# Kernel optimization log

Measured on AMD Instinct MI355X. Metric: run time of the kernel, lower is better.

The kernel has to match this reference:

```python
import jax, jax.numpy as jnp
import numpy as np

N = 50000       # nodes
E = 500000      # edges (before self-loops)
F_IN = 128      # node feature dim
F_E = 16        # edge feature dim
H = 8           # heads (conv1, conv2)
C1 = 32         # 256 // 8
C2 = 16         # 128 // 8
OUT = 1         # conv3 output channels (1 head, concat=False)
NS = 0.2        # leaky_relu negative slope
EPS = 1e-5      # batchnorm eps


def setup_inputs() -> dict:
    key = jax.random.key(0)
    ks = jax.random.split(key, 32)
    r = lambda k, s: jax.random.normal(k, s, jnp.float32) * 0.1
    inp = {
        'x': jax.random.normal(ks[0], (N, F_IN), jnp.float32),
        'edge_index': jax.random.randint(ks[1], (2, E), 0, N, jnp.int32),
        'edge_attr': jax.random.normal(ks[2], (E, F_E), jnp.float32),
        # conv1 (share_weights=True -> single lin)
        'W1': r(ks[3], (F_IN, H * C1)), 'b1': jnp.zeros((H * C1,), jnp.float32),
        'We1': r(ks[4], (F_E, H * C1)), 'att1': r(ks[5], (H, C1)),
        'bo1': jnp.zeros((H * C1,), jnp.float32),
        'g1': jnp.ones((H * C1,), jnp.float32), 'bt1': jnp.zeros((H * C1,), jnp.float32),
        # conv2 (share_weights=True)
        'W2': r(ks[6], (H * C1, H * C2)), 'b2': jnp.zeros((H * C2,), jnp.float32),
        'We2': r(ks[7], (F_E, H * C2)), 'att2': r(ks[8], (H, C2)),
        'bo2': jnp.zeros((H * C2,), jnp.float32),
        'g2': jnp.ones((H * C2,), jnp.float32), 'bt2': jnp.zeros((H * C2,), jnp.float32),
        # conv3 (share_weights=False -> separate lin_l / lin_r; 1 head, concat=False)
        'W3l': r(ks[9], (H * C2, OUT)), 'b3l': jnp.zeros((OUT,), jnp.float32),
        'W3r': r(ks[10], (H * C2, OUT)), 'b3r': jnp.zeros((OUT,), jnp.float32),
        'We3': r(ks[11], (F_E, OUT)), 'att3': r(ks[12], (1, OUT)),
        'bo3': jnp.zeros((OUT,), jnp.float32),
    }
    return inp


def _gatv2(x, src, dst, eattr, Wl, bl, Wr, br, We, att, bo, heads, ch, concat):
    """One GATv2Conv layer (PyG semantics), edges already include self-loops."""
    n = x.shape[0]
    xl = (x @ Wl + bl).reshape(n, heads, ch)              # source transform
    xr = (x @ Wr + br).reshape(n, heads, ch)              # target transform
    e = (eattr @ We).reshape(-1, heads, ch)               # edge transform (no bias)
    m = xl[src] + xr[dst] + e                             # [Etot, H, C]
    logit = jnp.einsum('ehc,hc->eh', jax.nn.leaky_relu(m, NS), att)
    lmax = jax.ops.segment_max(logit, dst, num_segments=n)
    ex = jnp.exp(logit - lmax[dst])
    denom = jax.ops.segment_sum(ex, dst, num_segments=n)
    alpha = ex / (denom[dst] + 1e-16)                     # segment softmax over dst
    out = jax.ops.segment_sum(alpha[:, :, None] * xl[src], dst, num_segments=n)
    out = out.reshape(n, heads * ch) if concat else out.mean(axis=1)
    return out + bo


def _bn(x, g, b):
    mu = x.mean(axis=0)
    var = ((x - mu) ** 2).mean(axis=0)
    return g * (x - mu) * jax.lax.rsqrt(var + EPS) + b


def reference(x, edge_index, edge_attr, W1, b1, We1, att1, bo1, g1, bt1,
              W2, b2, We2, att2, bo2, g2, bt2,
              W3l, b3l, W3r, b3r, We3, att3, bo3):
    n = x.shape[0]
    # add_self_loops=True with fill_value='mean' for edge_attr (PyG default)
    loop = jnp.arange(n, dtype=edge_index.dtype)
    src = jnp.concatenate([edge_index[0], loop])
    dst = jnp.concatenate([edge_index[1], loop])
    ea = jnp.concatenate([edge_attr,
                          jnp.broadcast_to(edge_attr.mean(axis=0), (n, edge_attr.shape[1]))], axis=0)

    h = _gatv2(x, src, dst, ea, W1, b1, W1, b1, We1, att1, bo1, H, C1, True)
    h = jax.nn.elu(_bn(h, g1, bt1))
    h = _gatv2(h, src, dst, ea, W2, b2, W2, b2, We2, att2, bo2, H, C2, True)
    h = jax.nn.elu(_bn(h, g2, bt2))
    out = _gatv2(h, src, dst, ea, W3l, b3l, W3r, b3r, We3, att3, bo3, 1, OUT, False)
    return out  # [N, 1]
```

## Files before the change

kernel.cpp:

```cpp
#include <hip/hip_runtime.h>

typedef unsigned short u16;
typedef __attribute__((ext_vector_type(4))) float f32x4;
typedef __attribute__((ext_vector_type(2))) float f32x2;
typedef __attribute__((ext_vector_type(8))) short bf16x8;

constexpr int Nn  = 50000;
constexpr int Ee  = 500000;
constexpr int ET  = Nn + Ee;
constexpr int FIN = 128;
constexpr int FE  = 16;
constexpr int Hh  = 8;
constexpr int C1  = 32, HC1 = 256;
constexpr int C2  = 16, HC2 = 128;
constexpr float NS  = 0.2f;
constexpr float EPS = 1e-5f;

__device__ __forceinline__ float b2f(u16 u) { return __uint_as_float(((unsigned)u) << 16); }
__device__ __forceinline__ u16 f2b(float f) {
  unsigned u = __float_as_uint(f);
  u += 0x7FFF + ((u >> 16) & 1);
  return (u16)(u >> 16);
}
__device__ __forceinline__ f32x2 ldbf2(const u16* p) {
  ushort2 u = *reinterpret_cast<const ushort2*>(p);
  return (f32x2){b2f(u.x), b2f(u.y)};
}
__device__ __forceinline__ void stbf2(u16* p, f32x2 v) {
  ushort2 u; u.x = f2b(v.x); u.y = f2b(v.y);
  *reinterpret_cast<ushort2*>(p) = u;
}

__global__ void k_init(int* __restrict__ deg, int* __restrict__ cursor, float* __restrict__ ea_mean,
                       float* __restrict__ bn1s, float* __restrict__ bn1q,
                       float* __restrict__ bn2s, float* __restrict__ bn2q) {
  int t = blockIdx.x * 256 + threadIdx.x;
  int stride = gridDim.x * 256;
  for (int i = t; i < Nn; i += stride) { deg[i] = 0; cursor[i] = 0; }
  if (t < FE) ea_mean[t] = 0.f;
  if (t >= 64 && t < 64 + HC1) { bn1s[t - 64] = 0.f; bn1q[t - 64] = 0.f; }
  if (t >= 384 && t < 384 + HC2) { bn2s[t - 384] = 0.f; bn2q[t - 384] = 0.f; }
}

__global__ void k_deg_mean(const int* __restrict__ ei, const float* __restrict__ ea,
                           int* __restrict__ deg, float* __restrict__ ea_mean) {
  int t = threadIdx.x;
  int e = blockIdx.x * 256 + t;
  if (e < ET) {
    int d = (e < Ee) ? ei[Ee + e] : (e - Ee);
    if ((unsigned)d >= (unsigned)Nn) d = 0;
    atomicAdd(&deg[d], 1);
  }
  __shared__ float s[256];
  int f  = t & 15;
  int r0 = (t >> 4) + blockIdx.x * 16;
  float acc = 0.f;
  for (int r = r0; r < Ee; r += gridDim.x * 16) acc += ea[r * FE + f];
  s[t] = acc;
  __syncthreads();
  if (t < 16) {
    float v = 0.f;
    for (int r = 0; r < 16; r++) v += s[r * 16 + t];
    atomicAdd(&ea_mean[t], v * (1.f / Ee));
  }
}

__global__ __launch_bounds__(1024) void k_scan(const int* __restrict__ deg, int* __restrict__ rowptr) {
  const int T = 1024;
  int t = threadIdx.x;
  const int CH = (Nn + T - 1) / T;
  int base = t * CH;
  int sum = 0;
  for (int i = 0; i < CH; i++) {
    int idx = base + i;
    if (idx < Nn) sum += deg[idx];
  }
  __shared__ int s[T];
  s[t] = sum;
  __syncthreads();
  for (int off = 1; off < T; off <<= 1) {
    int v = (t >= off) ? s[t - off] : 0;
    __syncthreads();
    s[t] += v;
    __syncthreads();
  }
  int run = (t == 0) ? 0 : s[t - 1];
  for (int i = 0; i < CH; i++) {
    int idx = base + i;
    if (idx < Nn) { rowptr[idx] = run; run += deg[idx]; }
  }
  if (t == T - 1) rowptr[Nn] = run;
}

__global__ void k_scatter(const int* __restrict__ ei, const int* __restrict__ rowptr,
                          int* __restrict__ cursor, int2* __restrict__ epack) {
  int e = blockIdx.x * 256 + threadIdx.x;
  if (e >= ET) return;
  int s, d;
  if (e < Ee) { s = ei[e]; d = ei[Ee + e]; } else { s = d = e - Ee; }
  if ((unsigned)s >= (unsigned)Nn) s = 0;
  if ((unsigned)d >= (unsigned)Nn) d = 0;
  int pos = rowptr[d] + atomicAdd(&cursor[d], 1);
  epack[pos] = make_int2(s, e);
}

__global__ void k_bn_coef(const float* __restrict__ sum, const float* __restrict__ sq,
                          const float* __restrict__ g, const float* __restrict__ bt,
                          float2* __restrict__ coef, int HC) {
  int ch = threadIdx.x;
  if (ch >= HC) return;
  float mu = sum[ch] * (1.f / Nn);
  float var = sq[ch] * (1.f / Nn) - mu * mu;
  float rs = rsqrtf(var + EPS);
  float sc = g[ch] * rs;
  coef[ch] = make_float2(sc, bt[ch] - sc * mu);
}

template <int HC>
__global__ void k_bn_stats(const u16* __restrict__ x, float* __restrict__ sum, float* __restrict__ sq) {
  long e0 = (long)blockIdx.x * 256 + threadIdx.x;
  long stride = (long)gridDim.x * 256;
  float s = 0.f, s2 = 0.f;
  for (long e = e0; e < (long)Nn * HC; e += stride) {
    float v = b2f(x[e]);
    s += v; s2 += v * v;
  }
  int ch = (int)(e0 % HC);
  atomicAdd(&sum[ch], s);
  atomicAdd(&sq[ch], s2);
}

template <int KK, int NN, typename AT, bool FUSE>
__global__ __launch_bounds__(256) void k_gemm_mfma(const AT* __restrict__ A, const float* __restrict__ W,
                                                   const float* __restrict__ bias, u16* __restrict__ C,
                                                   const float2* __restrict__ coef, int M) {
  constexpr int WT = KK + 8;
  __shared__ u16 Wt[64 * WT];
  int tid = threadIdx.x;
  int col0 = blockIdx.x * 64;
  int row0 = blockIdx.y * 64;
  for (int idx = tid; idx < KK * 64; idx += 256) {
    int k = idx >> 6, c = idx & 63;
    Wt[c * WT + k] = f2b(W[(size_t)k * NN + col0 + c]);
  }
  __syncthreads();
  int lane = tid & 63;
  int w = tid >> 6;
  int mr = lane & 15, quad = lane >> 4;
  int row = row0 + w * 16 + mr;
  f32x4 acc[4];
#pragma unroll
  for (int t = 0; t < 4; t++) acc[t] = (f32x4){0.f, 0.f, 0.f, 0.f};
  union Frag { bf16x8 v; u16 u[8]; };
  for (int kb = 0; kb < KK; kb += 32) {
    Frag a;
    if (row < M) {
      if constexpr (sizeof(AT) == 4) {
        const float* ap = (const float*)&A[(size_t)row * KK + kb + quad * 8];
        float4 a0 = *reinterpret_cast<const float4*>(ap);
        float4 a1 = *reinterpret_cast<const float4*>(ap + 4);
        a.u[0] = f2b(a0.x); a.u[1] = f2b(a0.y); a.u[2] = f2b(a0.z); a.u[3] = f2b(a0.w);
        a.u[4] = f2b(a1.x); a.u[5] = f2b(a1.y); a.u[6] = f2b(a1.z); a.u[7] = f2b(a1.w);
      } else {
        a.v = *reinterpret_cast<const bf16x8*>(&A[(size_t)row * KK + kb + quad * 8]);
        if constexpr (FUSE) {
          int k0 = kb + quad * 8;
#pragma unroll
          for (int j = 0; j < 8; j++) {
            float2 c2 = coef[k0 + j];
            float y = b2f(a.u[j]) * c2.x + c2.y;
            y = y > 0.f ? y : __expf(y) - 1.f;
            a.u[j] = f2b(y);
          }
        }
      }
    } else {
#pragma unroll
      for (int j = 0; j < 8; j++) a.u[j] = 0;
    }
#pragma unroll
    for (int t = 0; t < 4; t++) {
      const bf16x8* bp = reinterpret_cast<const bf16x8*>(&Wt[(t * 16 + mr) * WT + kb + quad * 8]);
      acc[t] = __builtin_amdgcn_mfma_f32_16x16x32_bf16(a.v, *bp, acc[t], 0, 0, 0);
    }
  }
  int orow = row0 + w * 16 + quad * 4;
#pragma unroll
  for (int t = 0; t < 4; t++) {
    int col = col0 + t * 16 + mr;
    float bs = bias[col];
#pragma unroll
    for (int r = 0; r < 4; r++) {
      int rr = orow + r;
      if (rr < M) C[(size_t)rr * NN + col] = f2b(acc[t][r] + bs);
    }
  }
}

template <int HC, int C, int WPN>
__global__ __launch_bounds__(256) void k_node_attn(
    const int* __restrict__ rowptr, const int2* __restrict__ epack,
    const u16* __restrict__ xl, const float* __restrict__ We, const float* __restrict__ att,
    const float* __restrict__ edge_attr, const float* __restrict__ ea_mean,
    const float* __restrict__ bo, u16* __restrict__ out) {
  int lane = threadIdx.x & 63;
  int gwid = (blockIdx.x << 2) + (threadIdx.x >> 6);
  int nwaves = gridDim.x << 2;
  int w = gwid % WPN;
  int i0 = gwid / WPN;
  int istride = nwaves / WPN;
  int c0 = w * 128 + lane * 2;
  f32x2 w2[FE];
#pragma unroll
  for (int k = 0; k < FE; k++) {
    float2 t = *reinterpret_cast<const float2*>(&We[k * HC + c0]);
    w2[k] = (f32x2){t.x, t.y};
  }
  float at0 = att[c0], at1 = att[c0 + 1];
  f32x2 ews2 = {0.f, 0.f};
#pragma unroll
  for (int k = 0; k < FE; k++) ews2 += ea_mean[k] * w2[k];
  float b0 = bo[c0], b1 = bo[c0 + 1];
  constexpr int RED = C / 2;
  constexpr int UN = 4;

  auto edge_ew = [&](int eid) -> f32x2 {
    if (eid < Ee) {
      const float4* ep = reinterpret_cast<const float4*>(&edge_attr[(size_t)eid * FE]);
      f32x2 a = {0.f, 0.f};
#pragma unroll
      for (int k4 = 0; k4 < 4; k4++) {
        float4 u = ep[k4];
        a += u.x * w2[4 * k4 + 0];
        a += u.y * w2[4 * k4 + 1];
        a += u.z * w2[4 * k4 + 2];
        a += u.w * w2[4 * k4 + 3];
      }
      return a;
    }
    return ews2;
  };

  for (int i = i0; i < Nn; i += istride) {
    int p0 = rowptr[i], p1 = rowptr[i + 1];
    f32x2 xd = ldbf2(&xl[(size_t)i * HC + c0]);
    float m = -1e30f, l = 0.f;
    f32x2 acc = {0.f, 0.f};
    int p = p0;
    for (; p + UN <= p1; p += UN) {
      int sA[UN], eA[UN];
#pragma unroll
      for (int j = 0; j < UN; j++) {
        int2 se = epack[p + j];
        sA[j] = __builtin_amdgcn_readfirstlane(se.x);
        eA[j] = __builtin_amdgcn_readfirstlane(se.y);
      }
      f32x2 xs[UN];
#pragma unroll
      for (int j = 0; j < UN; j++)
        xs[j] = ldbf2(&xl[(size_t)sA[j] * HC + c0]);
      f32x2 ew[UN];
#pragma unroll
      for (int j = 0; j < UN; j++) ew[j] = edge_ew(eA[j]);
      float part[UN];
#pragma unroll
      for (int j = 0; j < UN; j++) {
        f32x2 t = xs[j] + xd + ew[j];
        float t0 = t.x > 0.f ? t.x : NS * t.x;
        float t1 = t.y > 0.f ? t.y : NS * t.y;
        float pt = t0 * at0 + t1 * at1;
#pragma unroll
        for (int off = 1; off < RED; off <<= 1) pt += __shfl_xor(pt, off);
        part[j] = pt;
      }
      float mn = m;
#pragma unroll
      for (int j = 0; j < UN; j++) mn = fmaxf(mn, part[j]);
      float sc = __expf(m - mn);
      float a[UN], asum = 0.f;
      f32x2 ax = {0.f, 0.f};
#pragma unroll
      for (int j = 0; j < UN; j++) {
        a[j] = __expf(part[j] - mn);
        asum += a[j];
        ax += a[j] * xs[j];
      }
      l = l * sc + asum;
      acc = acc * sc + ax;
      m = mn;
    }
    for (; p < p1; p++) {
      int2 se = epack[p];
      int s = __builtin_amdgcn_readfirstlane(se.x);
      int eid = __builtin_amdgcn_readfirstlane(se.y);
      f32x2 ew = edge_ew(eid);
      f32x2 xs = ldbf2(&xl[(size_t)s * HC + c0]);
      f32x2 t = xs + xd + ew;
      float t0 = t.x > 0.f ? t.x : NS * t.x;
      float t1 = t.y > 0.f ? t.y : NS * t.y;
      float pt = t0 * at0 + t1 * at1;
#pragma unroll
      for (int off = 1; off < RED; off <<= 1) pt += __shfl_xor(pt, off);
      float mn = fmaxf(m, pt);
      float sc = __expf(m - mn);
      float a = __expf(pt - mn);
      l = l * sc + a;
      acc = acc * sc + a * xs;
      m = mn;
    }
    float inv = 1.f / (l + 1e-16f);
    f32x2 v = {acc.x * inv + b0, acc.y * inv + b1};
    stbf2(&out[(size_t)i * HC + c0], v);
  }
}

__global__ __launch_bounds__(256) void k_gemv3(const u16* __restrict__ h2,
                                               const float2* __restrict__ coef,
                                               const float* __restrict__ W3l, const float* __restrict__ b3l,
                                               const float* __restrict__ W3r, const float* __restrict__ b3r,
                                               float* __restrict__ xl3, float* __restrict__ xr3) {
  int lane = threadIdx.x & 63;
  int i = (blockIdx.x << 2) + (threadIdx.x >> 6);
  if (i >= Nn) return;
  float2 ca = coef[lane], cb = coef[64 + lane];
  float a = b2f(h2[(long)i * HC2 + lane]) * ca.x + ca.y;
  a = a > 0.f ? a : __expf(a) - 1.f;
  float b = b2f(h2[(long)i * HC2 + 64 + lane]) * cb.x + cb.y;
  b = b > 0.f ? b : __expf(b) - 1.f;
  float pl = a * W3l[lane] + b * W3l[64 + lane];
  float pr = a * W3r[lane] + b * W3r[64 + lane];
  for (int o = 1; o < 64; o <<= 1) { pl += __shfl_xor(pl, o); pr += __shfl_xor(pr, o); }
  if (lane == 0) { xl3[i] = pl + b3l[0]; xr3[i] = pr + b3r[0]; }
}

__global__ __launch_bounds__(256) void k_final3(
    const int* __restrict__ rowptr, const int2* __restrict__ epack,
    const float* __restrict__ xl3, const float* __restrict__ xr3,
    const float* __restrict__ We3, const float* __restrict__ att3,
    const float* __restrict__ edge_attr, const float* __restrict__ ea_mean,
    const float* __restrict__ bo3, float* __restrict__ out) {
  int lane = threadIdx.x & 63;
  int i = (blockIdx.x << 2) + (threadIdx.x >> 6);
  if (i >= Nn) return;
  float we[FE];
#pragma unroll
  for (int k4 = 0; k4 < 4; k4++) {
    float4 u = reinterpret_cast<const float4*>(We3)[k4];
    we[4 * k4] = u.x; we[4 * k4 + 1] = u.y; we[4 * k4 + 2] = u.z; we[4 * k4 + 3] = u.w;
  }
  float at = att3[0];
  float ews = 0.f;
#pragma unroll
  for (int k = 0; k < FE; k++) ews += ea_mean[k] * we[k];
  float xd = xr3[i];
  int p0 = rowptr[i], p1 = rowptr[i + 1];
  float m = -1e30f, l = 0.f, o = 0.f;
  for (int p = p0 + lane; p < p1; p += 64) {
    int2 se = epack[p];
    int s = se.x, eid = se.y;
    float ew;
    if (eid < Ee) {
      const float4* ep = reinterpret_cast<const float4*>(&edge_attr[(size_t)eid * FE]);
      ew = 0.f;
#pragma unroll
      for (int k4 = 0; k4 < 4; k4++) {
        float4 u = ep[k4];
        ew += u.x * we[4 * k4] + u.y * we[4 * k4 + 1] + u.z * we[4 * k4 + 2] + u.w * we[4 * k4 + 3];
      }
    } else ew = ews;
    float xsv = xl3[s];
    float t = xsv + xd + ew;
    float v = t > 0.f ? t : NS * t;
    float logit = v * at;
    float mn = fmaxf(m, logit);
    float sc = __expf(m - mn);
    float a = __expf(logit - mn);
    l = l * sc + a;
    o = o * sc + a * xsv;
    m = mn;
  }
  float M = m;
#pragma unroll
  for (int off = 1; off < 64; off <<= 1) M = fmaxf(M, __shfl_xor(M, off));
  float adj = __expf(m - M);
  float lw = l * adj, ow = o * adj;
#pragma unroll
  for (int off = 1; off < 64; off <<= 1) { lw += __shfl_xor(lw, off); ow += __shfl_xor(ow, off); }
  if (lane == 0) out[i] = ow / (lw + 1e-16f) + bo3[0];
}

extern "C" void kernel_launch(void* const* d_in, const int* in_sizes, int n_in,
                              void* d_out, int out_size, void* d_ws, size_t ws_size,
                              hipStream_t stream) {
  const float* x    = (const float*)d_in[0];
  const int*   ei   = (const int*)d_in[1];
  const float* ea   = (const float*)d_in[2];
  const float* W1   = (const float*)d_in[3];
  const float* b1   = (const float*)d_in[4];
  const float* We1  = (const float*)d_in[5];
  const float* att1 = (const float*)d_in[6];
  const float* bo1  = (const float*)d_in[7];
  const float* g1   = (const float*)d_in[8];
  const float* bt1  = (const float*)d_in[9];
  const float* W2   = (const float*)d_in[10];
  const float* b2   = (const float*)d_in[11];
  const float* We2  = (const float*)d_in[12];
  const float* att2 = (const float*)d_in[13];
  const float* bo2  = (const float*)d_in[14];
  const float* g2   = (const float*)d_in[15];
  const float* bt2  = (const float*)d_in[16];
  const float* W3l  = (const float*)d_in[17];
  const float* b3l  = (const float*)d_in[18];
  const float* W3r  = (const float*)d_in[19];
  const float* b3r  = (const float*)d_in[20];
  const float* We3  = (const float*)d_in[21];
  const float* att3 = (const float*)d_in[22];
  const float* bo3  = (const float*)d_in[23];
  float* out = (float*)d_out;

  char* ws = (char*)d_ws;
  size_t off = 0;
  auto alloc = [&](size_t bytes) -> void* {
    void* p = ws + off;
    off = (off + bytes + 255) & ~(size_t)255;
    return p;
  };
  int*    deg     = (int*)alloc((size_t)Nn * 4);
  int*    rowptr  = (int*)alloc((size_t)(Nn + 1) * 4);
  int*    cursor  = (int*)alloc((size_t)Nn * 4);
  int2*   epack   = (int2*)alloc((size_t)ET * 8);
  float*  ea_mean = (float*)alloc((size_t)FE * 4);
  float*  bn1s    = (float*)alloc(256 * 4);
  float*  bn1q    = (float*)alloc(256 * 4);
  float*  bn2s    = (float*)alloc(128 * 4);
  float*  bn2q    = (float*)alloc(128 * 4);
  float2* bncoef  = (float2*)alloc(256 * 8);
  float*  xl3     = (float*)alloc((size_t)Nn * 4);
  float*  xr3     = (float*)alloc((size_t)Nn * 4);
  u16*    xlA     = (u16*)alloc((size_t)Nn * 256 * 2);
  u16*    hB      = (u16*)alloc((size_t)Nn * 256 * 2);

  k_init<<<512, 256, 0, stream>>>(deg, cursor, ea_mean, bn1s, bn1q, bn2s, bn2q);
  k_deg_mean<<<(ET + 255) / 256, 256, 0, stream>>>(ei, ea, deg, ea_mean);
  k_scan<<<1, 1024, 0, stream>>>(deg, rowptr);
  k_scatter<<<(ET + 255) / 256, 256, 0, stream>>>(ei, rowptr, cursor, epack);

  k_gemm_mfma<FIN, HC1, float, false><<<dim3(HC1 / 64, (Nn + 63) / 64), 256, 0, stream>>>(
      x, W1, b1, xlA, nullptr, Nn);
  k_node_attn<HC1, C1, 2><<<2048, 256, 0, stream>>>(rowptr, epack, xlA, We1, att1,
                                                    ea, ea_mean, bo1, hB);
  k_bn_stats<HC1><<<256, 256, 0, stream>>>(hB, bn1s, bn1q);
  k_bn_coef<<<1, 256, 0, stream>>>(bn1s, bn1q, g1, bt1, bncoef, HC1);

  k_gemm_mfma<HC1, HC2, u16, true><<<dim3(HC2 / 64, (Nn + 63) / 64), 256, 0, stream>>>(
      hB, W2, b2, xlA, bncoef, Nn);
  k_node_attn<HC2, C2, 1><<<2048, 256, 0, stream>>>(rowptr, epack, xlA, We2, att2,
                                                    ea, ea_mean, bo2, hB);
  k_bn_stats<HC2><<<256, 256, 0, stream>>>(hB, bn2s, bn2q);
  k_bn_coef<<<1, 256, 0, stream>>>(bn2s, bn2q, g2, bt2, bncoef, HC2);

  k_gemv3<<<(Nn + 3) / 4, 256, 0, stream>>>(hB, bncoef, W3l, b3l, W3r, b3r, xl3, xr3);
  k_final3<<<(Nn + 3) / 4, 256, 0, stream>>>(rowptr, epack, xl3, xr3, We3, att3,
                                             ea, ea_mean, bo3, out);
}
```

Before: 756.3 us.

## Software-pipeline edge index loads and use DPP reductions in GAT aggregation

```diff
diff --git a/kernel.cpp b/kernel.cpp
--- a/kernel.cpp
+++ b/kernel.cpp
@@ -29,6 +29,16 @@
 __device__ __forceinline__ void stbf2(u16* p, f32x2 v) {
   ushort2 u; u.x = f2b(v.x); u.y = f2b(v.y);
   *reinterpret_cast<ushort2*>(p) = u;
+}
+
+template <int RED>
+__device__ __forceinline__ float red_sum(float v) {
+  v += __int_as_float(__builtin_amdgcn_update_dpp(0, __float_as_int(v), 0xB1, 0xF, 0xF, true));
+  v += __int_as_float(__builtin_amdgcn_update_dpp(0, __float_as_int(v), 0x4E, 0xF, 0xF, true));
+  v += __int_as_float(__builtin_amdgcn_update_dpp(0, __float_as_int(v), 0x141, 0xF, 0xF, true));
+  if constexpr (RED == 16)
+    v += __int_as_float(__builtin_amdgcn_update_dpp(0, __float_as_int(v), 0x140, 0xF, 0xF, true));
+  return v;
 }
 
 __global__ void k_init(int* __restrict__ deg, int* __restrict__ cursor, float* __restrict__ ea_mean,
@@ -241,37 +251,59 @@
     return ews2;
   };
 
-  for (int i = i0; i < Nn; i += istride) {
-    int p0 = rowptr[i], p1 = rowptr[i + 1];
-    f32x2 xd = ldbf2(&xl[(size_t)i * HC + c0]);
+  if (i0 >= Nn) return;
+  int p0 = rowptr[i0], p1 = rowptr[i0 + 1];
+  ushort2 xdr = *reinterpret_cast<const ushort2*>(&xl[(size_t)i0 * HC + c0]);
+
+  for (int i = i0; i < Nn;) {
+    int inext = i + istride;
+    int np0 = 0, np1 = 0;
+    ushort2 nxdr = make_ushort2(0, 0);
+    if (inext < Nn) {
+      np0 = rowptr[inext];
+      np1 = rowptr[inext + 1];
+      nxdr = *reinterpret_cast<const ushort2*>(&xl[(size_t)inext * HC + c0]);
+    }
+    f32x2 xd = (f32x2){b2f(xdr.x), b2f(xdr.y)};
+    int nb = (p1 - p0 + UN - 1) >> 2;
     float m = -1e30f, l = 0.f;
     f32x2 acc = {0.f, 0.f};
-    int p = p0;
-    for (; p + UN <= p1; p += UN) {
+
+    int2 se[UN];
+    int pb = p0;
+#pragma unroll
+    for (int j = 0; j < UN; j++) se[j] = epack[min(pb + j, p1 - 1)];
+
+    for (int b = 0; b < nb; b++) {
       int sA[UN], eA[UN];
 #pragma unroll
       for (int j = 0; j < UN; j++) {
-        int2 se = epack[p + j];
-        sA[j] = __builtin_amdgcn_readfirstlane(se.x);
-        eA[j] = __builtin_amdgcn_readfirstlane(se.y);
-      }
+        sA[j] = __builtin_amdgcn_readfirstlane(se[j].x);
+        eA[j] = __builtin_amdgcn_readfirstlane(se[j].y);
+      }
+      ushort2 xr[UN];
+#pragma unroll
+      for (int j = 0; j < UN; j++)
+        xr[j] = *reinterpret_cast<const ushort2*>(&xl[(size_t)sA[j] * HC + c0]);
+      int pn = pb + UN;
+      if (pn < p1) {
+#pragma unroll
+        for (int j = 0; j < UN; j++) se[j] = epack[min(pn + j, p1 - 1)];
+      }
+      f32x2 ew[UN];
+#pragma unroll
+      for (int j = 0; j < UN; j++) ew[j] = edge_ew(eA[j]);
       f32x2 xs[UN];
-#pragma unroll
-      for (int j = 0; j < UN; j++)
-        xs[j] = ldbf2(&xl[(size_t)sA[j] * HC + c0]);
-      f32x2 ew[UN];
-#pragma unroll
-      for (int j = 0; j < UN; j++) ew[j] = edge_ew(eA[j]);
       float part[UN];
 #pragma unroll
       for (int j = 0; j < UN; j++) {
+        xs[j] = (f32x2){b2f(xr[j].x), b2f(xr[j].y)};
         f32x2 t = xs[j] + xd + ew[j];
-        float t0 = t.x > 0.f ? t.x : NS * t.x;
-        float t1 = t.y > 0.f ? t.y : NS * t.y;
-        float pt = t0 * at0 + t1 * at1;
-#pragma unroll
-        for (int off = 1; off < RED; off <<= 1) pt += __shfl_xor(pt, off);
-        part[j] = pt;
+        f32x2 tn = t * NS;
+        f32x2 lk = {fmaxf(t.x, tn.x), fmaxf(t.y, tn.y)};
+        float pt = lk.x * at0 + lk.y * at1;
+        pt = red_sum<RED>(pt);
+        part[j] = (pb + j < p1) ? pt : -1e30f;
       }
       float mn = m;
 #pragma unroll
@@ -288,29 +320,12 @@
       l = l * sc + asum;
       acc = acc * sc + ax;
       m = mn;
-    }
-    for (; p < p1; p++) {
-      int2 se = epack[p];
-      int s = __builtin_amdgcn_readfirstlane(se.x);
-      int eid = __builtin_amdgcn_readfirstlane(se.y);
-      f32x2 ew = edge_ew(eid);
-      f32x2 xs = ldbf2(&xl[(size_t)s * HC + c0]);
-      f32x2 t = xs + xd + ew;
-      float t0 = t.x > 0.f ? t.x : NS * t.x;
-      float t1 = t.y > 0.f ? t.y : NS * t.y;
-      float pt = t0 * at0 + t1 * at1;
-#pragma unroll
-      for (int off = 1; off < RED; off <<= 1) pt += __shfl_xor(pt, off);
-      float mn = fmaxf(m, pt);
-      float sc = __expf(m - mn);
-      float a = __expf(pt - mn);
-      l = l * sc + a;
-      acc = acc * sc + a * xs;
-      m = mn;
+      pb = pn;
     }
     float inv = 1.f / (l + 1e-16f);
     f32x2 v = {acc.x * inv + b0, acc.y * inv + b1};
     stbf2(&out[(size_t)i * HC + c0], v);
+    i = inext; p0 = np0; p1 = np1; xdr = nxdr;
   }
 }
 
```

Result: faster. 729.0 us (-3.6%).
